# Kernel tuning notes

Hardware: AMD Instinct MI355X
Metric: run time of the kernel (lower is better)

Reference implementation:

```python
import jax, jax.numpy as jnp
import numpy as np

N_NODES = 100000
N_EMBED = 256
N_HIDDEN = 256
N_EDGES = 1600000


def setup_inputs() -> dict:
    key = jax.random.key(0)
    k_emb, k_w1, k_w2, k_ei = jax.random.split(key, 4)
    # Learned parameters. PyG ChebConv(K=1) holds one bias-free Linear per
    # Chebyshev order plus a shared bias; at K=1 that is a single W and b.
    emb = jax.random.normal(k_emb, (N_NODES, N_EMBED), dtype=jnp.float32)
    W1 = jax.random.normal(k_w1, (N_EMBED, N_HIDDEN), dtype=jnp.float32) * 0.05
    b1 = jnp.zeros((N_HIDDEN,), dtype=jnp.float32)
    W2 = jax.random.normal(k_w2, (N_HIDDEN, N_HIDDEN), dtype=jnp.float32) * 0.05
    b2 = jnp.zeros((N_HIDDEN,), dtype=jnp.float32)
    prop_edge_index = jax.random.randint(k_ei, (2, N_EDGES), 0, N_NODES, dtype=jnp.int64)
    return {"emb": emb, "W1": W1, "b1": b1, "W2": W2, "b2": b2,
            "prop_edge_index": prop_edge_index}


def reference(emb, W1, b1, W2, b2, prop_edge_index):
    # ChebConv with K=1: only Tx_0 = x is used, so each conv is x @ W + b.
    # edge_index affects only the (unused) Laplacian normalization at K=1.
    # Dropout is identity (training=False for a deterministic reference).
    x = jax.nn.relu(emb @ W1 + b1)          # [N, H] conv1 + ReLU
    out = x @ W2 + b2                        # [N, H] conv2
    return out
```

## Files before the change

kernel.cpp:

```cpp
#include <hip/hip_runtime.h>

#define M_NODES 100000
#define BM 128
#define NBLK ((M_NODES + BM - 1) / BM)

typedef float  f32x4  __attribute__((ext_vector_type(4)));
typedef short  bf16x8 __attribute__((ext_vector_type(8)));
typedef unsigned short u16x4 __attribute__((ext_vector_type(4)));

__device__ __forceinline__ unsigned short f2bf(float f) {
  union { float f; unsigned int u; } v; v.f = f;
  unsigned int u = v.u;
  return (unsigned short)((u + 0x7FFFu + ((u >> 16) & 1u)) >> 16);
}

__global__ void prep_w_kernel(const float* __restrict__ W1, const float* __restrict__ W2,
                              unsigned short* __restrict__ R1, unsigned short* __restrict__ R2) {
  int b = blockIdx.x;
  const float* W = (b < 64) ? W1 : W2;
  unsigned short* R = (b < 64) ? R1 : R2;
  int e  = ((b & 63) * 256 + (int)threadIdx.x) * 4;
  int n  = e >> 8;
  int k0 = e & 255;
  u16x4 h;
  #pragma unroll
  for (int i = 0; i < 4; ++i) h[i] = f2bf(W[(k0 + i) * 256 + n]);
  int kt = k0 >> 6, kl = k0 & 63;
  int off = kt * 16384 + n * 64 + (((kl >> 3) ^ (n & 7)) << 3) + (kl & 7);
  *(u16x4*)(R + off) = h;
}

__global__ __launch_bounds__(512, 2)
void cheb_fused(const float* __restrict__ X,
                const unsigned short* __restrict__ W1img,
                const unsigned short* __restrict__ W2img,
                const float* __restrict__ b1,
                const float* __restrict__ b2,
                float* __restrict__ out)
{
  __shared__ unsigned short lds[65536];
  unsigned short* Hbuf = lds;
  unsigned short* Ab0  = lds;
  unsigned short* Ab1  = lds + 8192;
  unsigned short* Wb0  = lds + 32768;
  unsigned short* Wb1  = lds + 49152;

  const int tid  = threadIdx.x;
  const int lane = tid & 63;
  const int w    = tid >> 6;
  const int wr   = w >> 2;
  const int wc   = w & 3;
  const int rb   = blockIdx.x;

  f32x4 acc[4][4] = {};
  f32x4 areg[4];

  auto stageW = [&](const unsigned short* img, int kt, unsigned short* dst) {
    const unsigned short* src = img + kt * 16384;
    #pragma unroll
    for (int it = 0; it < 4; ++it) {
      int chunk = it * 8 + w;
      __builtin_amdgcn_global_load_lds(
          (const __attribute__((address_space(1))) unsigned int*)(const void*)(src + chunk * 512 + lane * 8),
          (__attribute__((address_space(3))) unsigned int*)(void*)(dst + chunk * 512),
          16, 0, 0);
    }
  };
  auto loadA = [&](int kt) {
    #pragma unroll
    for (int i = 0; i < 4; ++i) {
      int e = (i * 512 + tid) * 4;
      int r = e >> 6, c = e & 63;
      int grow = rb * BM + r;
      f32x4 v = {0.f, 0.f, 0.f, 0.f};
      if (grow < M_NODES) v = *(const f32x4*)(X + (size_t)grow * 256 + kt * 64 + c);
      areg[i] = v;
    }
  };
  auto writeA = [&](unsigned short* dst) {
    #pragma unroll
    for (int i = 0; i < 4; ++i) {
      int e = (i * 512 + tid) * 4;
      int r = e >> 6, c = e & 63;
      u16x4 h;
      #pragma unroll
      for (int j = 0; j < 4; ++j) h[j] = f2bf(areg[i][j]);
      int off = r * 64 + (((c >> 3) ^ (r & 7)) << 3) + (c & 7);
      *(u16x4*)(dst + off) = h;
    }
  };
  auto compute = [&](const unsigned short* Abase, int rstride, int slotbase,
                     const unsigned short* B) {
    #pragma unroll
    for (int kk = 0; kk < 2; ++kk) {
      bf16x8 a[4], b[4];
      #pragma unroll
      for (int mi = 0; mi < 4; ++mi) {
        int r = wr * 64 + mi * 16 + (lane & 15);
        int slot = (slotbase + kk * 4 + (lane >> 4)) ^ (r & 7);
        a[mi] = *(const bf16x8*)(Abase + r * rstride + slot * 8);
      }
      #pragma unroll
      for (int ni = 0; ni < 4; ++ni) {
        int n = wc * 64 + ni * 16 + (lane & 15);
        int slot = (kk * 4 + (lane >> 4)) ^ (n & 7);
        b[ni] = *(const bf16x8*)(B + n * 64 + slot * 8);
      }
      #pragma unroll
      for (int mi = 0; mi < 4; ++mi)
        #pragma unroll
        for (int ni = 0; ni < 4; ++ni)
          acc[mi][ni] = __builtin_amdgcn_mfma_f32_16x16x32_bf16(a[mi], b[ni], acc[mi][ni], 0, 0, 0);
    }
  };

  loadA(0);
  stageW(W1img, 0, Wb0);
  writeA(Ab0);
  __syncthreads();

  #pragma unroll
  for (int kt = 0; kt < 4; ++kt) {
    unsigned short* Acur = (kt & 1) ? Ab1 : Ab0;
    unsigned short* Anxt = (kt & 1) ? Ab0 : Ab1;
    unsigned short* Wcur = (kt & 1) ? Wb1 : Wb0;
    unsigned short* Wnxt = (kt & 1) ? Wb0 : Wb1;
    if (kt < 3) {
      loadA(kt + 1);
      stageW(W1img, kt + 1, Wnxt);
    } else {
      stageW(W2img, 0, Wnxt);
    }
    compute(Acur, 64, 0, Wcur);
    if (kt < 3) writeA(Anxt);
    __syncthreads();
  }

  {
    float bn[4];
    #pragma unroll
    for (int ni = 0; ni < 4; ++ni) bn[ni] = b1[wc * 64 + ni * 16 + (lane & 15)];
    #pragma unroll
    for (int mi = 0; mi < 4; ++mi)
      #pragma unroll
      for (int ni = 0; ni < 4; ++ni) {
        int k = wc * 64 + ni * 16 + (lane & 15);
        #pragma unroll
        for (int rg = 0; rg < 4; ++rg) {
          int r = wr * 64 + mi * 16 + (lane >> 4) * 4 + rg;
          float v = fmaxf(acc[mi][ni][rg] + bn[ni], 0.f);
          int off = r * 256 + (((k >> 3) ^ (r & 7)) << 3) + (k & 7);
          Hbuf[off] = f2bf(v);
          acc[mi][ni][rg] = 0.f;
        }
      }
  }
  __syncthreads();

  #pragma unroll
  for (int kt = 0; kt < 4; ++kt) {
    unsigned short* Wcur = (kt & 1) ? Wb1 : Wb0;
    unsigned short* Wnxt = (kt & 1) ? Wb0 : Wb1;
    if (kt < 3) stageW(W2img, kt + 1, Wnxt);
    compute(Hbuf, 256, kt * 8, Wcur);
    if (kt < 3) __syncthreads();
  }

  {
    float bn[4];
    #pragma unroll
    for (int ni = 0; ni < 4; ++ni) bn[ni] = b2[wc * 64 + ni * 16 + (lane & 15)];
    #pragma unroll
    for (int mi = 0; mi < 4; ++mi)
      #pragma unroll
      for (int rg = 0; rg < 4; ++rg) {
        int r = wr * 64 + mi * 16 + (lane >> 4) * 4 + rg;
        int grow = rb * BM + r;
        if (grow < M_NODES) {
          #pragma unroll
          for (int ni = 0; ni < 4; ++ni) {
            int col = wc * 64 + ni * 16 + (lane & 15);
            out[(size_t)grow * 256 + col] = acc[mi][ni][rg] + bn[ni];
          }
        }
      }
  }
}

extern "C" void kernel_launch(void* const* d_in, const int* in_sizes, int n_in,
                              void* d_out, int out_size, void* d_ws, size_t ws_size,
                              hipStream_t stream) {
  const float* emb = (const float*)d_in[0];
  const float* W1  = (const float*)d_in[1];
  const float* b1  = (const float*)d_in[2];
  const float* W2  = (const float*)d_in[3];
  const float* b2  = (const float*)d_in[4];
  float* out = (float*)d_out;

  unsigned short* Wr1 = (unsigned short*)d_ws;
  unsigned short* Wr2 = Wr1 + 65536;

  prep_w_kernel<<<128, 256, 0, stream>>>(W1, W2, Wr1, Wr2);
  cheb_fused<<<NBLK, 512, 0, stream>>>(emb, Wr1, Wr2, b1, b2, out);
}
```

Baseline: 74.86 us.

## Load MFMA operands directly from global memory and shrink tile to 64 rows

Drops the LDS staging and double-buffering of X and the weights. Each wave now loads its X fragments straight from global memory into registers, converts them with packed bf16 instructions, and reads weight fragments from a plain transposed bf16 copy that stays in L2. The row tile is halved to 64 with 256-thread blocks, so LDS holds only the hidden activation and more blocks can be resident per CU. Outputs are written with nontemporal stores. In exchange, each weight fragment is re-read from L2 by every block, the X loads are strided per lane, and there is no explicit prefetch to overlap memory with MFMA.

```diff
diff --git a/kernel.cpp b/kernel.cpp
--- a/kernel.cpp
+++ b/kernel.cpp
@@ -1,12 +1,11 @@
 #include <hip/hip_runtime.h>
 
 #define M_NODES 100000
-#define BM 128
+#define BM 64
 #define NBLK ((M_NODES + BM - 1) / BM)
 
 typedef float  f32x4  __attribute__((ext_vector_type(4)));
 typedef short  bf16x8 __attribute__((ext_vector_type(8)));
-typedef unsigned short u16x4 __attribute__((ext_vector_type(4)));
 
 __device__ __forceinline__ unsigned short f2bf(float f) {
   union { float f; unsigned int u; } v; v.f = f;
@@ -14,176 +13,124 @@
   return (unsigned short)((u + 0x7FFFu + ((u >> 16) & 1u)) >> 16);
 }
 
-__global__ void prep_w_kernel(const float* __restrict__ W1, const float* __restrict__ W2,
-                              unsigned short* __restrict__ R1, unsigned short* __restrict__ R2) {
-  int b = blockIdx.x;
-  const float* W = (b < 64) ? W1 : W2;
-  unsigned short* R = (b < 64) ? R1 : R2;
-  int e  = ((b & 63) * 256 + (int)threadIdx.x) * 4;
-  int n  = e >> 8;
-  int k0 = e & 255;
-  u16x4 h;
-  #pragma unroll
-  for (int i = 0; i < 4; ++i) h[i] = f2bf(W[(k0 + i) * 256 + n]);
-  int kt = k0 >> 6, kl = k0 & 63;
-  int off = kt * 16384 + n * 64 + (((kl >> 3) ^ (n & 7)) << 3) + (kl & 7);
-  *(u16x4*)(R + off) = h;
+__device__ __forceinline__ bf16x8 cvt8(f32x4 u0, f32x4 u1) {
+  union { unsigned int u[4]; bf16x8 v; } r;
+  asm("v_cvt_pk_bf16_f32 %0, %1, %2" : "=v"(r.u[0]) : "v"(u0[0]), "v"(u0[1]));
+  asm("v_cvt_pk_bf16_f32 %0, %1, %2" : "=v"(r.u[1]) : "v"(u0[2]), "v"(u0[3]));
+  asm("v_cvt_pk_bf16_f32 %0, %1, %2" : "=v"(r.u[2]) : "v"(u1[0]), "v"(u1[1]));
+  asm("v_cvt_pk_bf16_f32 %0, %1, %2" : "=v"(r.u[3]) : "v"(u1[2]), "v"(u1[3]));
+  return r.v;
 }
 
-__global__ __launch_bounds__(512, 2)
+__global__ void prep_w(const float* __restrict__ W1, const float* __restrict__ W2,
+                       unsigned short* __restrict__ U1, unsigned short* __restrict__ U2) {
+  int b = blockIdx.x;
+  const float* W = (b < 256) ? W1 : W2;
+  unsigned short* U = (b < 256) ? U1 : U2;
+  int n = b & 255, k = threadIdx.x;
+  U[n * 256 + k] = f2bf(W[k * 256 + n]);
+}
+
+__global__ __launch_bounds__(256, 4)
 void cheb_fused(const float* __restrict__ X,
-                const unsigned short* __restrict__ W1img,
-                const unsigned short* __restrict__ W2img,
+                const unsigned short* __restrict__ W1u,
+                const unsigned short* __restrict__ W2u,
                 const float* __restrict__ b1,
                 const float* __restrict__ b2,
                 float* __restrict__ out)
 {
-  __shared__ unsigned short lds[65536];
-  unsigned short* Hbuf = lds;
-  unsigned short* Ab0  = lds;
-  unsigned short* Ab1  = lds + 8192;
-  unsigned short* Wb0  = lds + 32768;
-  unsigned short* Wb1  = lds + 49152;
+  __shared__ unsigned short Hbuf[64 * 256];
 
   const int tid  = threadIdx.x;
   const int lane = tid & 63;
-  const int w    = tid >> 6;
-  const int wr   = w >> 2;
-  const int wc   = w & 3;
+  const int l15  = lane & 15;
+  const int lhi  = lane >> 4;
+  const int wc   = tid >> 6;
   const int rb   = blockIdx.x;
 
   f32x4 acc[4][4] = {};
-  f32x4 areg[4];
 
-  auto stageW = [&](const unsigned short* img, int kt, unsigned short* dst) {
-    const unsigned short* src = img + kt * 16384;
+  #pragma unroll 1
+  for (int kk = 0; kk < 8; ++kk) {
+    const int kof = kk * 32 + lhi * 8;
+    bf16x8 a[4], b[4];
     #pragma unroll
-    for (int it = 0; it < 4; ++it) {
-      int chunk = it * 8 + w;
-      __builtin_amdgcn_global_load_lds(
-          (const __attribute__((address_space(1))) unsigned int*)(const void*)(src + chunk * 512 + lane * 8),
-          (__attribute__((address_space(3))) unsigned int*)(void*)(dst + chunk * 512),
-          16, 0, 0);
+    for (int mi = 0; mi < 4; ++mi) {
+      int grow = rb * BM + mi * 16 + l15;
+      f32x4 u0 = {0.f, 0.f, 0.f, 0.f}, u1 = {0.f, 0.f, 0.f, 0.f};
+      if (grow < M_NODES) {
+        const float* p = X + (size_t)grow * 256 + kof;
+        u0 = *(const f32x4*)p;
+        u1 = *(const f32x4*)(p + 4);
+      }
+      a[mi] = cvt8(u0, u1);
     }
-  };
-  auto loadA = [&](int kt) {
     #pragma unroll
-    for (int i = 0; i < 4; ++i) {
-      int e = (i * 512 + tid) * 4;
-      int r = e >> 6, c = e & 63;
-      int grow = rb * BM + r;
-      f32x4 v = {0.f, 0.f, 0.f, 0.f};
-      if (grow < M_NODES) v = *(const f32x4*)(X + (size_t)grow * 256 + kt * 64 + c);
-      areg[i] = v;
+    for (int ni = 0; ni < 4; ++ni) {
+      int n = wc * 64 + ni * 16 + l15;
+      b[ni] = *(const bf16x8*)(W1u + n * 256 + kof);
     }
-  };
-  auto writeA = [&](unsigned short* dst) {
     #pragma unroll
-    for (int i = 0; i < 4; ++i) {
-      int e = (i * 512 + tid) * 4;
-      int r = e >> 6, c = e & 63;
-      u16x4 h;
+    for (int mi = 0; mi < 4; ++mi)
       #pragma unroll
-      for (int j = 0; j < 4; ++j) h[j] = f2bf(areg[i][j]);
-      int off = r * 64 + (((c >> 3) ^ (r & 7)) << 3) + (c & 7);
-      *(u16x4*)(dst + off) = h;
-    }
-  };
-  auto compute = [&](const unsigned short* Abase, int rstride, int slotbase,
-                     const unsigned short* B) {
+      for (int ni = 0; ni < 4; ++ni)
+        acc[mi][ni] = __builtin_amdgcn_mfma_f32_16x16x32_bf16(a[mi], b[ni], acc[mi][ni], 0, 0, 0);
+  }
+
+  {
     #pragma unroll
-    for (int kk = 0; kk < 2; ++kk) {
-      bf16x8 a[4], b[4];
-      #pragma unroll
-      for (int mi = 0; mi < 4; ++mi) {
-        int r = wr * 64 + mi * 16 + (lane & 15);
-        int slot = (slotbase + kk * 4 + (lane >> 4)) ^ (r & 7);
-        a[mi] = *(const bf16x8*)(Abase + r * rstride + slot * 8);
-      }
-      #pragma unroll
-      for (int ni = 0; ni < 4; ++ni) {
-        int n = wc * 64 + ni * 16 + (lane & 15);
-        int slot = (kk * 4 + (lane >> 4)) ^ (n & 7);
-        b[ni] = *(const bf16x8*)(B + n * 64 + slot * 8);
-      }
+    for (int ni = 0; ni < 4; ++ni) {
+      int k = wc * 64 + ni * 16 + l15;
+      float bn = b1[k];
       #pragma unroll
       for (int mi = 0; mi < 4; ++mi)
         #pragma unroll
-        for (int ni = 0; ni < 4; ++ni)
-          acc[mi][ni] = __builtin_amdgcn_mfma_f32_16x16x32_bf16(a[mi], b[ni], acc[mi][ni], 0, 0, 0);
+        for (int rg = 0; rg < 4; ++rg) {
+          int r = mi * 16 + lhi * 4 + rg;
+          float v = fmaxf(acc[mi][ni][rg] + bn, 0.f);
+          Hbuf[r * 256 + (((k >> 3) ^ (r & 7)) << 3) + (k & 7)] = f2bf(v);
+          acc[mi][ni][rg] = 0.f;
+        }
     }
-  };
-
-  loadA(0);
-  stageW(W1img, 0, Wb0);
-  writeA(Ab0);
+  }
   __syncthreads();
 
-  #pragma unroll
-  for (int kt = 0; kt < 4; ++kt) {
-    unsigned short* Acur = (kt & 1) ? Ab1 : Ab0;
-    unsigned short* Anxt = (kt & 1) ? Ab0 : Ab1;
-    unsigned short* Wcur = (kt & 1) ? Wb1 : Wb0;
-    unsigned short* Wnxt = (kt & 1) ? Wb0 : Wb1;
-    if (kt < 3) {
-      loadA(kt + 1);
-      stageW(W1img, kt + 1, Wnxt);
-    } else {
-      stageW(W2img, 0, Wnxt);
+  #pragma unroll 1
+  for (int kk = 0; kk < 8; ++kk) {
+    bf16x8 a[4], b[4];
+    #pragma unroll
+    for (int mi = 0; mi < 4; ++mi) {
+      int r = mi * 16 + l15;
+      int kslot = (kk * 4 + lhi) ^ (r & 7);
+      a[mi] = *(const bf16x8*)(Hbuf + r * 256 + (kslot << 3));
     }
-    compute(Acur, 64, 0, Wcur);
-    if (kt < 3) writeA(Anxt);
-    __syncthreads();
+    #pragma unroll
+    for (int ni = 0; ni < 4; ++ni) {
+      int n = wc * 64 + ni * 16 + l15;
+      b[ni] = *(const bf16x8*)(W2u + n * 256 + kk * 32 + lhi * 8);
+    }
+    #pragma unroll
+    for (int mi = 0; mi < 4; ++mi)
+      #pragma unroll
+      for (int ni = 0; ni < 4; ++ni)
+        acc[mi][ni] = __builtin_amdgcn_mfma_f32_16x16x32_bf16(a[mi], b[ni], acc[mi][ni], 0, 0, 0);
   }
 
   {
-    float bn[4];
     #pragma unroll
-    for (int ni = 0; ni < 4; ++ni) bn[ni] = b1[wc * 64 + ni * 16 + (lane & 15)];
-    #pragma unroll
-    for (int mi = 0; mi < 4; ++mi)
+    for (int ni = 0; ni < 4; ++ni) {
+      int col = wc * 64 + ni * 16 + l15;
+      float bn = b2[col];
       #pragma unroll
-      for (int ni = 0; ni < 4; ++ni) {
-        int k = wc * 64 + ni * 16 + (lane & 15);
+      for (int mi = 0; mi < 4; ++mi)
         #pragma unroll
         for (int rg = 0; rg < 4; ++rg) {
-          int r = wr * 64 + mi * 16 + (lane >> 4) * 4 + rg;
-          float v = fmaxf(acc[mi][ni][rg] + bn[ni], 0.f);
-          int off = r * 256 + (((k >> 3) ^ (r & 7)) << 3) + (k & 7);
-          Hbuf[off] = f2bf(v);
-          acc[mi][ni][rg] = 0.f;
+          int grow = rb * BM + mi * 16 + lhi * 4 + rg;
+          if (grow < M_NODES)
+            __builtin_nontemporal_store(acc[mi][ni][rg] + bn,
+                                        out + (size_t)grow * 256 + col);
         }
-      }
-  }
-  __syncthreads();
-
-  #pragma unroll
-  for (int kt = 0; kt < 4; ++kt) {
-    unsigned short* Wcur = (kt & 1) ? Wb1 : Wb0;
-    unsigned short* Wnxt = (kt & 1) ? Wb0 : Wb1;
-    if (kt < 3) stageW(W2img, kt + 1, Wnxt);
-    compute(Hbuf, 256, kt * 8, Wcur);
-    if (kt < 3) __syncthreads();
-  }
-
-  {
-    float bn[4];
-    #pragma unroll
-    for (int ni = 0; ni < 4; ++ni) bn[ni] = b2[wc * 64 + ni * 16 + (lane & 15)];
-    #pragma unroll
-    for (int mi = 0; mi < 4; ++mi)
-      #pragma unroll
-      for (int rg = 0; rg < 4; ++rg) {
-        int r = wr * 64 + mi * 16 + (lane >> 4) * 4 + rg;
-        int grow = rb * BM + r;
-        if (grow < M_NODES) {
-          #pragma unroll
-          for (int ni = 0; ni < 4; ++ni) {
-            int col = wc * 64 + ni * 16 + (lane & 15);
-            out[(size_t)grow * 256 + col] = acc[mi][ni][rg] + bn[ni];
-          }
-        }
-      }
+    }
   }
 }
 
@@ -197,9 +144,9 @@
   const float* b2  = (const float*)d_in[4];
   float* out = (float*)d_out;
 
-  unsigned short* Wr1 = (unsigned short*)d_ws;
-  unsigned short* Wr2 = Wr1 + 65536;
+  unsigned short* U1 = (unsigned short*)d_ws;
+  unsigned short* U2 = U1 + 65536;
 
-  prep_w_kernel<<<128, 256, 0, stream>>>(W1, W2, Wr1, Wr2);
-  cheb_fused<<<NBLK, 512, 0, stream>>>(emb, Wr1, Wr2, b1, b2, out);
+  prep_w<<<512, 256, 0, stream>>>(W1, W2, U1, U2);
+  cheb_fused<<<NBLK, 256, 0, stream>>>(emb, U1, U2, b1, b2, out);
 }
```

After: 136.0 us. +81.7%, slower.
